# Kernel tuning notes

Hardware: AMD Instinct MI355X
Metric: run time of the kernel (lower is better)

## Reference

```python
import jax, jax.numpy as jnp
import numpy as np

ALPHA = 0.2  # LeakyReLU negative slope


def setup_inputs() -> dict:
    key = jax.random.key(0)
    k1, k2, k3, k4 = jax.random.split(key, 4)
    bs, L, D, F_in, F_out = 8, 4096, 16, 128, 128
    x = jax.random.normal(k1, (bs, L, F_in), dtype=jnp.float32)
    adj = jax.random.randint(k2, (bs, L, D), 0, L, dtype=jnp.int64)
    # xavier_normal-ish init for params
    W = jax.random.normal(k3, (F_in, F_out), dtype=jnp.float32) * (1.414 * (2.0 / (F_in + F_out)) ** 0.5)
    a = jax.random.normal(k4, (2 * F_out, 1), dtype=jnp.float32) * (1.414 * (2.0 / (2 * F_out + 1)) ** 0.5)
    return {"x": x, "adj": adj, "W": W, "a": a}


def reference(x, adj, W, a):
    # x: [B, L, F_in], adj: [B, L, D] int node indices, W: [F_in, F_out], a: [2*F_out, 1]
    # Project first, then gather (same math as gather-then-project, fewer FLOPs).
    h = jnp.matmul(x, W)                                  # [B, L, F_out]
    h_prime = jax.vmap(lambda hb, ab: hb[ab])(h, adj)     # [B, L, D, F_out]
    # h_node: neighbor-0 features broadcast over D (torch repeat_interleave of h_prime[:,:,0:1,:])
    h_node = jnp.broadcast_to(h_prime[:, :, :1, :], h_prime.shape)
    # attention logits: concat(h_prime, h_node) @ a -> [B, L, D, 1]
    e = jnp.concatenate([h_prime, h_node], axis=-1) @ a
    e = jnp.where(e > 0, e, ALPHA * e)                    # LeakyReLU
    attn = jax.nn.softmax(e[..., 0], axis=-1)             # softmax over neighbors D -> [B, L, D]
    # dropout is identity in eval mode (p=0.0)
    out = jnp.einsum('bld,bldf->blf', attn, h_prime)      # weighted aggregate -> [B, L, F_out]
    return jax.nn.elu(out)                                # concat=True branch
```

## Files before the change

kernel.cpp:

```cpp
#include <hip/hip_runtime.h>
#include <hip/hip_bf16.h>

#define BATCH 8
#define SEQ   4096
#define DEG   16
#define FD    128
#define NTOT  (BATCH * SEQ)
#define ALPHA 0.2f
#define LDS_WK 132

typedef __attribute__((ext_vector_type(8))) short short8v;
typedef __attribute__((ext_vector_type(4))) short short4v;
typedef __attribute__((ext_vector_type(4))) float float4v;
typedef __attribute__((ext_vector_type(4))) float f32x4;
typedef __attribute__((ext_vector_type(4))) unsigned int u32x4;

__device__ __forceinline__ unsigned short f2bf(float f) {
    unsigned int u = __float_as_uint(f);
    u += 0x7fffu + ((u >> 16) & 1u);
    return (unsigned short)(u >> 16);
}

__global__ __launch_bounds__(256) void gat_proj(
    const float* __restrict__ x, const float* __restrict__ W,
    const float* __restrict__ avec, unsigned short* __restrict__ hb,
    float2* __restrict__ s12)
{
    __shared__ unsigned short Wt[128 * LDS_WK];

    const int t = threadIdx.x;
    const int bid = blockIdx.x;
    const int xcd = bid & 7, blk = bid >> 3;
    const long long rowBase = (long long)xcd * SEQ + (long long)blk * 64;

    {
        const int q = t & 31;
        const int kh = t >> 5;
        #pragma unroll
        for (int j = 0; j < 8; ++j) {
            const int kp = kh + 8 * j;
            const f32x4 w0 = *reinterpret_cast<const f32x4*>(&W[(2 * kp) * FD + 4 * q]);
            const f32x4 w1 = *reinterpret_cast<const f32x4*>(&W[(2 * kp + 1) * FD + 4 * q]);
            #pragma unroll
            for (int e2 = 0; e2 < 4; ++e2) {
                const unsigned int pk = (unsigned int)f2bf(w0[e2])
                                      | ((unsigned int)f2bf(w1[e2]) << 16);
                *reinterpret_cast<unsigned int*>(&Wt[(4 * q + e2) * LDS_WK + 2 * kp]) = pk;
            }
        }
    }

    const int lane = t & 63, wv = t >> 6;
    const int g = lane >> 4, mrow = lane & 15;
    const long long row = rowBase + wv * 16 + mrow;
    short8v afrag[4];
    {
        const float* xr = x + row * FD + 4 * g;
        #pragma unroll
        for (int kb = 0; kb < 4; ++kb) {
            const f32x4 x0 = __builtin_nontemporal_load(
                reinterpret_cast<const f32x4*>(xr + 32 * kb));
            const f32x4 x1 = __builtin_nontemporal_load(
                reinterpret_cast<const f32x4*>(xr + 32 * kb + 16));
            short8v f;
            f[0] = (short)f2bf(x0[0]); f[1] = (short)f2bf(x0[1]);
            f[2] = (short)f2bf(x0[2]); f[3] = (short)f2bf(x0[3]);
            f[4] = (short)f2bf(x1[0]); f[5] = (short)f2bf(x1[1]);
            f[6] = (short)f2bf(x1[2]); f[7] = (short)f2bf(x1[3]);
            afrag[kb] = f;
        }
    }
    __syncthreads();

    float4v acc[8];
    #pragma unroll
    for (int tn = 0; tn < 8; ++tn) { acc[tn][0] = 0.f; acc[tn][1] = 0.f; acc[tn][2] = 0.f; acc[tn][3] = 0.f; }

    #pragma unroll
    for (int tn = 0; tn < 8; ++tn) {
        const int nbase = (16 * tn + mrow) * LDS_WK + 4 * g;
        #pragma unroll
        for (int kb = 0; kb < 4; ++kb) {
            const short4v lo = *reinterpret_cast<const short4v*>(&Wt[nbase + 32 * kb]);
            const short4v hi = *reinterpret_cast<const short4v*>(&Wt[nbase + 32 * kb + 16]);
            short8v bf;
            bf[0] = lo[0]; bf[1] = lo[1]; bf[2] = lo[2]; bf[3] = lo[3];
            bf[4] = hi[0]; bf[5] = hi[1]; bf[6] = hi[2]; bf[7] = hi[3];
            acc[tn] = __builtin_amdgcn_mfma_f32_16x16x32_bf16(afrag[kb], bf, acc[tn], 0, 0, 0);
        }
    }

    float s1p[4] = {0.f, 0.f, 0.f, 0.f};
    float s2p[4] = {0.f, 0.f, 0.f, 0.f};
    #pragma unroll
    for (int tn = 0; tn < 8; ++tn) {
        const int col = mrow + 16 * tn;
        const float a1 = avec[col], a2 = avec[FD + col];
        #pragma unroll
        for (int r = 0; r < 4; ++r) {
            const float v = acc[tn][r];
            hb[(rowBase + wv * 16 + 4 * g + r) * FD + col] = f2bf(v);
            s1p[r] = fmaf(v, a1, s1p[r]);
            s2p[r] = fmaf(v, a2, s2p[r]);
        }
    }
    #pragma unroll
    for (int mo = 1; mo < 16; mo <<= 1) {
        #pragma unroll
        for (int r = 0; r < 4; ++r) {
            s1p[r] += __shfl_xor(s1p[r], mo, 64);
            s2p[r] += __shfl_xor(s2p[r], mo, 64);
        }
    }
    if (mrow == 0) {
        #pragma unroll
        for (int r = 0; r < 4; ++r)
            s12[rowBase + wv * 16 + 4 * g + r] = make_float2(s1p[r], s2p[r]);
    }
}

__global__ __launch_bounds__(256) void gat_aggr(
    const int* __restrict__ adj, const unsigned short* __restrict__ hb,
    const float2* __restrict__ s12, float* __restrict__ out)
{
    const int t = threadIdx.x;
    const int wv = t >> 6;
    const int lane = t & 63;
    const int g = lane >> 4, c = lane & 15;
    const int bid = blockIdx.x;
    const int xcd = bid & 7, blk = bid >> 3;
    const long long node = (long long)xcd * SEQ + (long long)blk * 4 + wv;
    const long long bBase = (long long)xcd * SEQ;

    const int* ap = adj + node * DEG;
    const int nbc = ap[c];
    int nbr[4];
    #pragma unroll
    for (int i = 0; i < 4; ++i) nbr[i] = ap[g + 4 * i];

    const float2 sv = s12[bBase + nbc];
    const float s2n0 = __shfl(sv.y, 0, 64);
    float ev = sv.x + s2n0;
    ev = ev > 0.f ? ev : ALPHA * ev;
    float p = __expf(ev);
    float sum = p;
    #pragma unroll
    for (int mo = 1; mo < 16; mo <<= 1) sum += __shfl_xor(sum, mo, 64);
    const float pn = p * (1.f / sum);

    float accv[8] = {0.f, 0.f, 0.f, 0.f, 0.f, 0.f, 0.f, 0.f};
    #pragma unroll
    for (int i = 0; i < 4; ++i) {
        const float ai = __shfl(pn, g + 4 * i, 64);
        const u32x4* rp = reinterpret_cast<const u32x4*>(
            hb + ((bBase + (long long)nbr[i]) << 7));
        const u32x4 u = rp[c];
        #pragma unroll
        for (int j = 0; j < 4; ++j) {
            const unsigned int w = u[j];
            accv[2 * j]     = fmaf(ai, __uint_as_float(w << 16), accv[2 * j]);
            accv[2 * j + 1] = fmaf(ai, __uint_as_float(w & 0xffff0000u), accv[2 * j + 1]);
        }
    }
    #pragma unroll
    for (int j = 0; j < 8; ++j) {
        accv[j] += __shfl_xor(accv[j], 16, 64);
        accv[j] += __shfl_xor(accv[j], 32, 64);
        accv[j] = accv[j] > 0.f ? accv[j] : (__expf(accv[j]) - 1.f);
    }
    if (lane < 32) {
        f32x4 o;
        if (g == 0) { o[0] = accv[0]; o[1] = accv[1]; o[2] = accv[2]; o[3] = accv[3]; }
        else        { o[0] = accv[4]; o[1] = accv[5]; o[2] = accv[6]; o[3] = accv[7]; }
        __builtin_nontemporal_store(o, reinterpret_cast<f32x4*>(
            out + node * FD + c * 8 + g * 4));
    }
}

extern "C" void kernel_launch(void* const* d_in, const int* in_sizes, int n_in,
                              void* d_out, int out_size, void* d_ws, size_t ws_size,
                              hipStream_t stream) {
    const float* x  = (const float*)d_in[0];
    const int* adj  = (const int*)d_in[1];
    const float* W  = (const float*)d_in[2];
    const float* a  = (const float*)d_in[3];
    float* out = (float*)d_out;

    unsigned short* hb = (unsigned short*)d_ws;
    float2* s12 = (float2*)((char*)d_ws + (size_t)NTOT * FD * 2);

    gat_proj<<<dim3(NTOT / 64), dim3(256), 0, stream>>>(x, W, a, hb, s12);
    gat_aggr<<<dim3(NTOT / 4), dim3(256), 0, stream>>>(adj, hb, s12, out);
}
```

Baseline: 24.56 us.

## Transpose projection MFMA for packed stores and restructure aggregation lane mapping

In the projection kernel, the MFMA operands are swapped so each lane holds four consecutive output features of one node. This allows packed 8-byte bf16 stores and a two-step shuffle reduction for the attention scores, replacing scattered 2-byte stores and a 4-level shuffle tree. The aggregation kernel now gives each lane two features of all 16 neighbors: neighbor indices are loaded uniformly, weights are broadcast with readlane, and the cross-group shuffle reduction disappears. The trade-off is 16 serial 4-byte gathers per lane instead of 4 wider 16-byte gathers, which may raise memory latency exposure.

```diff
diff --git a/kernel.cpp b/kernel.cpp
--- a/kernel.cpp
+++ b/kernel.cpp
@@ -13,7 +13,7 @@
 typedef __attribute__((ext_vector_type(4))) short short4v;
 typedef __attribute__((ext_vector_type(4))) float float4v;
 typedef __attribute__((ext_vector_type(4))) float f32x4;
-typedef __attribute__((ext_vector_type(4))) unsigned int u32x4;
+typedef __attribute__((ext_vector_type(2))) float f32x2;
 
 __device__ __forceinline__ unsigned short f2bf(float f) {
     unsigned int u = __float_as_uint(f);
@@ -52,10 +52,10 @@
 
     const int lane = t & 63, wv = t >> 6;
     const int g = lane >> 4, mrow = lane & 15;
-    const long long row = rowBase + wv * 16 + mrow;
-    short8v afrag[4];
+    const long long node = rowBase + wv * 16 + mrow;
+    short8v xfrag[4];
     {
-        const float* xr = x + row * FD + 4 * g;
+        const float* xr = x + node * FD + 4 * g;
         #pragma unroll
         for (int kb = 0; kb < 4; ++kb) {
             const f32x4 x0 = __builtin_nontemporal_load(
@@ -67,7 +67,7 @@
             f[2] = (short)f2bf(x0[2]); f[3] = (short)f2bf(x0[3]);
             f[4] = (short)f2bf(x1[0]); f[5] = (short)f2bf(x1[1]);
             f[6] = (short)f2bf(x1[2]); f[7] = (short)f2bf(x1[3]);
-            afrag[kb] = f;
+            xfrag[kb] = f;
         }
     }
     __syncthreads();
@@ -83,40 +83,34 @@
         for (int kb = 0; kb < 4; ++kb) {
             const short4v lo = *reinterpret_cast<const short4v*>(&Wt[nbase + 32 * kb]);
             const short4v hi = *reinterpret_cast<const short4v*>(&Wt[nbase + 32 * kb + 16]);
-            short8v bf;
-            bf[0] = lo[0]; bf[1] = lo[1]; bf[2] = lo[2]; bf[3] = lo[3];
-            bf[4] = hi[0]; bf[5] = hi[1]; bf[6] = hi[2]; bf[7] = hi[3];
-            acc[tn] = __builtin_amdgcn_mfma_f32_16x16x32_bf16(afrag[kb], bf, acc[tn], 0, 0, 0);
+            short8v wf;
+            wf[0] = lo[0]; wf[1] = lo[1]; wf[2] = lo[2]; wf[3] = lo[3];
+            wf[4] = hi[0]; wf[5] = hi[1]; wf[6] = hi[2]; wf[7] = hi[3];
+            acc[tn] = __builtin_amdgcn_mfma_f32_16x16x32_bf16(wf, xfrag[kb], acc[tn], 0, 0, 0);
         }
     }
 
-    float s1p[4] = {0.f, 0.f, 0.f, 0.f};
-    float s2p[4] = {0.f, 0.f, 0.f, 0.f};
+    float s1p = 0.f, s2p = 0.f;
     #pragma unroll
     for (int tn = 0; tn < 8; ++tn) {
-        const int col = mrow + 16 * tn;
-        const float a1 = avec[col], a2 = avec[FD + col];
+        const int col = 16 * tn + 4 * g;
+        const unsigned int u0 = (unsigned int)f2bf(acc[tn][0])
+                              | ((unsigned int)f2bf(acc[tn][1]) << 16);
+        const unsigned int u1 = (unsigned int)f2bf(acc[tn][2])
+                              | ((unsigned int)f2bf(acc[tn][3]) << 16);
+        *reinterpret_cast<uint2*>(&hb[node * FD + col]) = make_uint2(u0, u1);
+        const f32x4 a1 = *reinterpret_cast<const f32x4*>(&avec[col]);
+        const f32x4 a2 = *reinterpret_cast<const f32x4*>(&avec[FD + col]);
         #pragma unroll
         for (int r = 0; r < 4; ++r) {
-            const float v = acc[tn][r];
-            hb[(rowBase + wv * 16 + 4 * g + r) * FD + col] = f2bf(v);
-            s1p[r] = fmaf(v, a1, s1p[r]);
-            s2p[r] = fmaf(v, a2, s2p[r]);
+            s1p = fmaf(acc[tn][r], a1[r], s1p);
+            s2p = fmaf(acc[tn][r], a2[r], s2p);
         }
     }
-    #pragma unroll
-    for (int mo = 1; mo < 16; mo <<= 1) {
-        #pragma unroll
-        for (int r = 0; r < 4; ++r) {
-            s1p[r] += __shfl_xor(s1p[r], mo, 64);
-            s2p[r] += __shfl_xor(s2p[r], mo, 64);
-        }
-    }
-    if (mrow == 0) {
-        #pragma unroll
-        for (int r = 0; r < 4; ++r)
-            s12[rowBase + wv * 16 + 4 * g + r] = make_float2(s1p[r], s2p[r]);
-    }
+    s1p += __shfl_xor(s1p, 16, 64);  s2p += __shfl_xor(s2p, 16, 64);
+    s1p += __shfl_xor(s1p, 32, 64);  s2p += __shfl_xor(s2p, 32, 64);
+    if (lane < 16)
+        s12[rowBase + wv * 16 + lane] = make_float2(s1p, s2p);
 }
 
 __global__ __launch_bounds__(256) void gat_aggr(
@@ -124,57 +118,46 @@
     const float2* __restrict__ s12, float* __restrict__ out)
 {
     const int t = threadIdx.x;
-    const int wv = t >> 6;
     const int lane = t & 63;
-    const int g = lane >> 4, c = lane & 15;
+    const int wv_u = __builtin_amdgcn_readfirstlane(t) >> 6;
     const int bid = blockIdx.x;
     const int xcd = bid & 7, blk = bid >> 3;
-    const long long node = (long long)xcd * SEQ + (long long)blk * 4 + wv;
-    const long long bBase = (long long)xcd * SEQ;
+    const int node = xcd * SEQ + blk * 4 + wv_u;
+    const int bBase = xcd * SEQ;
 
     const int* ap = adj + node * DEG;
+    int nb[16];
+    #pragma unroll
+    for (int d = 0; d < 16; ++d) nb[d] = ap[d];
+
+    const int c = lane & 15;
     const int nbc = ap[c];
-    int nbr[4];
-    #pragma unroll
-    for (int i = 0; i < 4; ++i) nbr[i] = ap[g + 4 * i];
-
-    const float2 sv = s12[bBase + nbc];
-    const float s2n0 = __shfl(sv.y, 0, 64);
-    float ev = sv.x + s2n0;
+    const float s2n0 = s12[bBase + nb[0]].y;
+    float ev = s12[bBase + nbc].x + s2n0;
     ev = ev > 0.f ? ev : ALPHA * ev;
     float p = __expf(ev);
     float sum = p;
     #pragma unroll
     for (int mo = 1; mo < 16; mo <<= 1) sum += __shfl_xor(sum, mo, 64);
-    const float pn = p * (1.f / sum);
+    p *= 1.f / sum;
 
-    float accv[8] = {0.f, 0.f, 0.f, 0.f, 0.f, 0.f, 0.f, 0.f};
+    float a0 = 0.f, a1 = 0.f;
     #pragma unroll
-    for (int i = 0; i < 4; ++i) {
-        const float ai = __shfl(pn, g + 4 * i, 64);
-        const u32x4* rp = reinterpret_cast<const u32x4*>(
-            hb + ((bBase + (long long)nbr[i]) << 7));
-        const u32x4 u = rp[c];
-        #pragma unroll
-        for (int j = 0; j < 4; ++j) {
-            const unsigned int w = u[j];
-            accv[2 * j]     = fmaf(ai, __uint_as_float(w << 16), accv[2 * j]);
-            accv[2 * j + 1] = fmaf(ai, __uint_as_float(w & 0xffff0000u), accv[2 * j + 1]);
-        }
+    for (int d = 0; d < 16; ++d) {
+        const float pd = __uint_as_float(
+            __builtin_amdgcn_readlane(__float_as_uint(p), d));
+        const unsigned int* rp = reinterpret_cast<const unsigned int*>(
+            hb + (((long long)(bBase + nb[d])) << 7));
+        const unsigned int u = rp[lane];
+        a0 = fmaf(pd, __uint_as_float(u << 16), a0);
+        a1 = fmaf(pd, __uint_as_float(u & 0xffff0000u), a1);
     }
-    #pragma unroll
-    for (int j = 0; j < 8; ++j) {
-        accv[j] += __shfl_xor(accv[j], 16, 64);
-        accv[j] += __shfl_xor(accv[j], 32, 64);
-        accv[j] = accv[j] > 0.f ? accv[j] : (__expf(accv[j]) - 1.f);
-    }
-    if (lane < 32) {
-        f32x4 o;
-        if (g == 0) { o[0] = accv[0]; o[1] = accv[1]; o[2] = accv[2]; o[3] = accv[3]; }
-        else        { o[0] = accv[4]; o[1] = accv[5]; o[2] = accv[6]; o[3] = accv[7]; }
-        __builtin_nontemporal_store(o, reinterpret_cast<f32x4*>(
-            out + node * FD + c * 8 + g * 4));
-    }
+
+    f32x2 o;
+    o[0] = a0 > 0.f ? a0 : (__expf(a0) - 1.f);
+    o[1] = a1 > 0.f ? a1 : (__expf(a1) - 1.f);
+    __builtin_nontemporal_store(o, reinterpret_cast<f32x2*>(
+        out + (long long)node * FD + lane * 2));
 }
 
 extern "C" void kernel_launch(void* const* d_in, const int* in_sizes, int n_in,
```

Result: faster. 23.01 us (-6.3%).
